# Kernel optimization log

Measured on AMD Instinct MI355X. Metric: run time of the kernel, lower is better.

Reference implementation:

```python
import jax, jax.numpy as jnp
import numpy as np
from itertools import combinations

A = 4          # anchor_points
K = 16         # neighbor_num
INTRA = A * (A - 1) // 2   # 6
CH = INTRA * 2 + A * A     # 28 = generator channels
B, N, S = 1, 8192, 4096
CIN, COUT = 64, 128


def cdist(x):
    # pairwise euclidean distances [B,N,N], zero-safe sqrt (zero grad at d=0)
    sq = jnp.sum(x * x, -1)
    d2 = sq[:, :, None] + sq[:, None, :] - 2.0 * jnp.einsum('bnc,bmc->bnm', x, x)
    d2 = jnp.maximum(d2, 0.0)
    m = d2 > 0
    return jnp.where(m, jnp.sqrt(jnp.where(m, d2, 1.0)), 0.0)


def index_points(points, idx):
    # points [B,N,...], idx [B,*] -> [B,*,...]
    return jax.vmap(lambda p, i: p[i])(points, idx)


def index_points_dists(dists, i1, i2):
    # dists [B,N,N]; result[b,...] = dists[b, i1[b,...], i2[b,...]]
    i1, i2 = jnp.broadcast_arrays(i1, i2)
    return jax.vmap(lambda d, a, b: d[a, b])(dists, i1, i2)


def generator(xyz):
    # RotationInvariantDistFea.forward(xyz, concat_raw_relative_fea=True)
    D = cdist(xyz)
    neg_nd, ni = jax.lax.top_k(-D, K)   # K >= A; smallest-K, sorted ascending
    nd = -neg_nd
    ai = ni[:, :, :A]
    # intra-anchor dists: dists to anchors 1..A-1 plus pairwise dists among them
    subs = [index_points_dists(D, ai[:, :, pi], ai[:, :, pj])[:, :, None]
            for pi, pj in combinations(range(1, A), 2)]
    intra = jnp.concatenate([nd[:, :, 1:A]] + subs, axis=2)  # [B,P,6]
    # inter-anchor dists: center anchors x neighbor anchors -> [B,P,K,A*A]
    nai = index_points(ai, ni)                                # [B,P,K,A]
    inter = index_points_dists(D, ai[:, :, None, :, None],
                               nai[:, :, :, None, :]).reshape(D.shape[0], D.shape[1], K, A * A)
    center = jnp.broadcast_to(intra[:, :, None, :], (intra.shape[0], intra.shape[1], K, INTRA))
    rf = jnp.concatenate([center, index_points(intra, ni), inter], axis=3)  # [B,P,K,28]
    return rf, ni, D


def mlp(x, W, b, g, be, act):
    # Linear + BatchNorm1d (training mode: stats over batch*points) + optional leaky_relu(0.2)
    y = x @ W + b
    mu = jnp.mean(y, (0, 1))
    var = jnp.var(y, (0, 1))
    y = (y - mu) * jax.lax.rsqrt(var + 1e-5) * g + be
    return jax.nn.leaky_relu(y, 0.2) if act else y


def forward(xyz, feature, sample_indexes, Ww, bw, gw, betaw, Wb, bb, gb, betab, Wo, bo, go, betao):
    rf_before, ni_before, D_before = generator(xyz)
    intra_before = rf_before[:, :, 0, :INTRA]
    xyz_s = index_points(xyz, sample_indexes)
    feat = index_points(feature, sample_indexes)
    intra_before = index_points(intra_before, sample_indexes)
    rf_after, ni_after, _ = generator(xyz_s)
    intra_after = rf_after[:, :, 0, :INTRA]
    a_before = index_points(ni_before[:, :, :A], sample_indexes)                  # [B,S,A]
    a_after = jax.vmap(lambda s, a: s[a])(sample_indexes, ni_after[:, :, :A])     # map to global idx
    inter = index_points_dists(D_before, a_before[:, :, :, None],
                               a_after[:, :, None, :]).reshape(B, S, A * A)
    adf = jnp.concatenate([intra_before, intra_after, inter], axis=2)             # [B,S,28]
    w = mlp(adf, Ww, bw, gw, betaw, False)
    bia = mlp(adf, Wb, bb, gb, betab, False)
    feat = jax.nn.leaky_relu(feat * w + bia, 0.2)
    feat = jnp.concatenate([feat, adf], axis=2)                                   # [B,S,92]
    feat = mlp(feat, Wo, bo, go, betao, True)                                     # [B,S,128]
    return xyz_s, feat, rf_after, ni_after


def setup_inputs():
    key = jax.random.key(0)
    ks = jax.random.split(key, 8)
    xyz = jax.random.normal(ks[0], (B, N, 3), jnp.float32)
    feature = jax.random.normal(ks[1], (B, N, CIN), jnp.float32)
    sample_indexes = jnp.stack([jax.random.permutation(jax.random.fold_in(ks[2], i), N)[:S]
                                for i in range(B)]).astype(jnp.int32)

    def lin(k, cin, cout):
        k1, k2 = jax.random.split(k)
        W = jax.random.normal(k1, (cin, cout), jnp.float32) / np.float32(np.sqrt(cin))
        b = jax.random.normal(k2, (cout,), jnp.float32) * 0.01
        return W, b, jnp.ones((cout,), jnp.float32), jnp.zeros((cout,), jnp.float32)

    Ww, bw, gw, betaw = lin(ks[5], CH, CIN)
    Wb, bb, gb, betab = lin(ks[6], CH, CIN)
    Wo, bo, go, betao = lin(ks[7], CH + CIN, COUT)
    return dict(xyz=xyz, feature=feature, sample_indexes=sample_indexes,
                Ww=Ww, bw=bw, gw=gw, betaw=betaw,
                Wb=Wb, bb=bb, gb=gb, betab=betab,
                Wo=Wo, bo=bo, go=go, betao=betao)


def reference(xyz, feature, sample_indexes, Ww, bw, gw, betaw, Wb, bb, gb, betab, Wo, bo, go, betao):
    return forward(xyz, feature, sample_indexes, Ww, bw, gw, betaw, Wb, bb, gb, betab, Wo, bo, go, betao)
```

## Files before the change

kernel.cpp:

```cpp
#include <hip/hip_runtime.h>
#include <hip/hip_bf16.h>
#include <math.h>

#define N_PTS 8192
#define S_PTS 4096
typedef unsigned long long u64;
typedef unsigned u32;

__device__ __forceinline__ float pair_dist_d(const float4 a, const float4 b) {
    double ax = a.x, ay = a.y, az = a.z;
    double bx = b.x, by = b.y, bz = b.z;
    double dx = ax - bx, dy = ay - by, dz = az - bz;
    double d2 = dx * dx + dy * dy + dz * dz;
    return d2 > 0.0 ? (float)sqrt(d2) : 0.0f;
}

__device__ __forceinline__ float d2_f32_gram(const float4 a, const float4 b) {
    float dot = __fadd_rn(__fadd_rn(__fmul_rn(a.x, b.x), __fmul_rn(a.y, b.y)),
                          __fmul_rn(a.z, b.z));
    float d2 = __fsub_rn(__fadd_rn(a.w, b.w), __fmul_rn(2.0f, dot));
    return fmaxf(d2, 0.0f);
}

__global__ __launch_bounds__(256) void stage_kernel(
        const float* __restrict__ xyz, const int* __restrict__ sidx,
        float4* __restrict__ cb, float4* __restrict__ ca,
        float* __restrict__ out_xyz_s) {
    int i = blockIdx.x * blockDim.x + threadIdx.x;
    if (i < N_PTS) {
        float x = xyz[i * 3 + 0], y = xyz[i * 3 + 1], z = xyz[i * 3 + 2];
        float sq = __fadd_rn(__fadd_rn(__fmul_rn(x, x), __fmul_rn(y, y)),
                             __fmul_rn(z, z));
        cb[i] = make_float4(x, y, z, sq);
    }
    if (i < S_PTS) {
        int si = sidx[i];
        float x = xyz[si * 3 + 0], y = xyz[si * 3 + 1], z = xyz[si * 3 + 2];
        float sq = __fadd_rn(__fadd_rn(__fmul_rn(x, x), __fmul_rn(y, y)),
                             __fmul_rn(z, z));
        ca[i] = make_float4(x, y, z, sq);
        out_xyz_s[i * 3 + 0] = x;
        out_xyz_s[i * 3 + 1] = y;
        out_xyz_s[i * 3 + 2] = z;
    }
}


template <int KOUT, int ITERS>
__device__ u64 knn_full_ladder(const float4 q, const float4* __restrict__ cand,
                               int lane) {
    u32 Lk[KOUT], Li[KOUT];
#pragma unroll
    for (int j = 0; j < KOUT; ++j) { Lk[j] = 0xFFFFFFFFu; Li[j] = 0xFFFFFFFFu; }
    int c = lane;
    for (int tt = 0; tt < ITERS; ++tt, c += 64) {
        float d2 = d2_f32_gram(q, cand[c]);
        float Df = d2 > 0.0f ? __fsqrt_rn(d2) : 0.0f;
        u32 kb = __float_as_uint(Df);
        if (kb < Lk[KOUT - 1]) {
#pragma unroll
            for (int j = KOUT - 1; j >= 1; --j) {
                bool up = kb < Lk[j - 1], ins = kb < Lk[j];
                Lk[j] = up ? Lk[j - 1] : (ins ? kb : Lk[j]);
                Li[j] = up ? Li[j - 1] : (ins ? (u32)c : Li[j]);
            }
            bool i0 = kb < Lk[0];
            Lk[0] = i0 ? kb : Lk[0];
            Li[0] = i0 ? (u32)c : Li[0];
        }
    }
    u64 Lu[KOUT];
#pragma unroll
    for (int j = 0; j < KOUT; ++j) Lu[j] = ((u64)Lk[j] << 32) | (u64)Li[j];
    u64 res = ~0ull;
#pragma unroll
    for (int r = 0; r < KOUT; ++r) {
        u64 m = Lu[0];
#pragma unroll
        for (int off = 32; off >= 1; off >>= 1) {
            u64 o = __shfl_xor(m, off, 64);
            m = (o < m) ? o : m;
        }
        if (lane == r) res = m;
        if (Lu[0] == m) {
#pragma unroll
            for (int j = 0; j < KOUT - 1; ++j) Lu[j] = Lu[j + 1];
            Lu[KOUT - 1] = ~0ull;
        }
    }
    return res;
}

template <int J, int K, int NC>
__device__ u64 knn_select(const float4 q, const float4* __restrict__ cand,
                          int t, u32* mins, u64* buf, u32* shm) {
    int lane = t & 63, wid = t >> 6;
    u32 d2b[J];
    u32 m = 0xFFFFFFFFu;
#pragma unroll
    for (int j = 0; j < J; ++j) {
        float d2 = d2_f32_gram(q, cand[t + 256 * j]);
        u32 b = __float_as_uint(d2);
        d2b[j] = b;
        m = b < m ? b : m;
    }
    mins[t] = m;
    __syncthreads();
    if (wid == 0) {
        u32 v = mins[lane];
        u32 v2 = mins[lane + 64];  v = v2 < v ? v2 : v;
        v2 = mins[lane + 128];     v = v2 < v ? v2 : v;
        v2 = mins[lane + 192];     v = v2 < v ? v2 : v;
#pragma unroll
        for (int k = 2; k <= 64; k <<= 1) {
#pragma unroll
            for (int j2 = k >> 1; j2 >= 1; j2 >>= 1) {
                u32 o = __shfl_xor(v, j2, 64);
                bool keepMin = (((lane & j2) == 0) == ((lane & k) == 0));
                bool less = o < v;
                v = keepMin ? (less ? o : v) : (less ? v : o);
            }
        }
        if (lane == K - 1) shm[0] = v;
    }
    __syncthreads();
    u32 tau = shm[0];
    u32 c = 0;
#pragma unroll
    for (int j = 0; j < J; ++j) c += (d2b[j] <= tau) ? 1u : 0u;
    u32 x = c;
#pragma unroll
    for (int off = 1; off < 64; off <<= 1) {
        u32 y = __shfl_up(x, off, 64);
        if (lane >= off) x += y;
    }
    if (lane == 63) shm[1 + wid] = x;
    __syncthreads();
    u32 base = x - c;
    for (int w = 0; w < wid; ++w) base += shm[1 + w];
    u32 cnt = shm[1] + shm[2] + shm[3] + shm[4];
    if (cnt <= 256u) {
        u32 off = base;
#pragma unroll
        for (int j = 0; j < J; ++j) {
            if (d2b[j] <= tau) {
                float d2 = __uint_as_float(d2b[j]);
                float D = d2 > 0.0f ? __fsqrt_rn(d2) : 0.0f;
                buf[off++] = ((u64)__float_as_uint(D) << 32) |
                             (u64)(u32)(t + 256 * j);
            }
        }
    }
    __syncthreads();
    u64 res = ~0ull;
    if (wid == 0) {
        if (cnt <= 64u) {
            u64 v = (lane < (int)cnt) ? buf[lane] : ~0ull;
#pragma unroll
            for (int k = 2; k <= 64; k <<= 1) {
#pragma unroll
                for (int j2 = k >> 1; j2 >= 1; j2 >>= 1) {
                    u64 o = __shfl_xor(v, j2, 64);
                    bool keepMin = (((lane & j2) == 0) == ((lane & k) == 0));
                    bool less = o < v;
                    v = keepMin ? (less ? o : v) : (less ? v : o);
                }
            }
            res = v;
        } else if (cnt <= 256u) {
            u64 L0 = ~0ull, L1 = ~0ull, L2 = ~0ull, L3 = ~0ull;
            for (u32 mm = lane; mm < cnt; mm += 64) {
                u64 kk = buf[mm];
                if (kk < L3) {
                    if (kk < L1) {
                        L3 = L2; L2 = L1;
                        if (kk < L0) { L1 = L0; L0 = kk; } else L1 = kk;
                    } else {
                        if (kk < L2) { L3 = L2; L2 = kk; } else L3 = kk;
                    }
                }
            }
#pragma unroll
            for (int r = 0; r < K; ++r) {
                u64 mr = L0;
#pragma unroll
                for (int off = 32; off >= 1; off >>= 1) {
                    u64 o = __shfl_xor(mr, off, 64);
                    mr = (o < mr) ? o : mr;
                }
                if (lane == r) res = mr;
                if (L0 == mr) { L0 = L1; L1 = L2; L2 = L3; L3 = ~0ull; }
            }
        } else {
            res = knn_full_ladder<K, NC / 64>(q, cand, lane);
        }
    }
    return res;
}

__global__ __launch_bounds__(256, 4) void knn_kernel(
        const float4* __restrict__ cb, const float4* __restrict__ ca,
        const int* __restrict__ sidx,
        int* __restrict__ a_before, float* __restrict__ intra_before,
        int* __restrict__ ni_i, float* __restrict__ intra_after,
        float* __restrict__ out_ni) {
    __shared__ u32 mins[256];
    __shared__ u64 buf[256];
    __shared__ u32 shm[8];
    int t = threadIdx.x, lane = t & 63, wid = t >> 6;
    int bid = blockIdx.x;
    if (bid < S_PTS) {
        int s = bid;
        float4 q = ca[s];
        u64 res = knn_select<16, 16, 4096>(q, ca, t, mins, buf, shm);
        if (wid == 0) {
            int idx = (int)(res & 0xffffffffull);
            if (lane < 16) {
                ni_i[s * 16 + lane] = idx;
                out_ni[s * 16 + lane] = (float)idx;
            }
            if (lane >= 1 && lane < 4)
                intra_after[s * 6 + (lane - 1)] = pair_dist_d(q, ca[idx]);
            int i1 = __shfl(idx, 1, 64);
            int i2 = __shfl(idx, 2, 64);
            int i3 = __shfl(idx, 3, 64);
            if (lane < 3) {
                int pa = (lane == 2) ? i2 : i1;
                int pb = (lane == 0) ? i2 : i3;
                intra_after[s * 6 + 3 + lane] = pair_dist_d(ca[pa], ca[pb]);
            }
        }
    } else {
        int s = bid - S_PTS;
        float4 q = cb[sidx[s]];
        u64 res = knn_select<32, 4, 8192>(q, cb, t, mins, buf, shm);
        if (wid == 0) {
            int idx = (int)(res & 0xffffffffull);
            if (lane < 4) a_before[s * 4 + lane] = idx;
            if (lane >= 1 && lane < 4)
                intra_before[s * 6 + (lane - 1)] = pair_dist_d(q, cb[idx]);
            int i1 = __shfl(idx, 1, 64);
            int i2 = __shfl(idx, 2, 64);
            int i3 = __shfl(idx, 3, 64);
            if (lane < 3) {
                int pa = (lane == 2) ? i2 : i1;
                int pb = (lane == 0) ? i2 : i3;
                intra_before[s * 6 + 3 + lane] = pair_dist_d(cb[pa], cb[pb]);
            }
        }
    }
}

__global__ __launch_bounds__(256) void assemble_kernel(
        const float4* __restrict__ ca, const float4* __restrict__ cb,
        const int* __restrict__ ni_i, const float* __restrict__ intra_after,
        const int* __restrict__ a_before, const float* __restrict__ intra_before,
        const int* __restrict__ sidx,
        float* __restrict__ out_rf, float* __restrict__ adf) {
    __shared__ int s_ni[4][16];
    __shared__ float s_rf[4][16 * 28];
    __shared__ float s_ia[4][8];
    int t = threadIdx.x, wid = t >> 6, lane = t & 63;
    int s = blockIdx.x * 4 + wid;
    if (lane < 16) s_ni[wid][lane] = ni_i[s * 16 + lane];
    if (lane < 6) s_ia[wid][lane] = intra_after[s * 6 + lane];
    __syncthreads();

    int k = lane >> 2, qq = lane & 3;
    int nai_q = ni_i[s_ni[wid][k] * 16 + qq];
    float4 pq = ca[nai_q];
#pragma unroll
    for (int p = 0; p < 4; ++p) {
        float4 pp = ca[s_ni[wid][p]];
        s_rf[wid][k * 28 + 12 + p * 4 + qq] = pair_dist_d(pp, pq);
    }
    for (int idx = lane; idx < 16 * 12; idx += 64) {
        int kk = idx / 12, c = idx % 12;
        float v = (c < 6) ? s_ia[wid][c] : intra_after[s_ni[wid][kk] * 6 + (c - 6)];
        s_rf[wid][kk * 28 + c] = v;
    }
    if (lane < 16) {
        int p = lane >> 2, q2 = lane & 3;
        int ib = a_before[s * 4 + p];
        int ia = sidx[s_ni[wid][q2]];
        adf[s * 28 + 12 + lane] = pair_dist_d(cb[ib], cb[ia]);
    } else if (lane >= 32 && lane < 38) {
        adf[s * 28 + (lane - 32)] = intra_before[s * 6 + (lane - 32)];
    } else if (lane >= 40 && lane < 46) {
        adf[s * 28 + 6 + (lane - 40)] = s_ia[wid][lane - 40];
    }
    __syncthreads();
    const int base = s * 16 * 28;
    for (int idx = lane; idx < 16 * 28; idx += 64) out_rf[base + idx] = s_rf[wid][idx];
}

__global__ __launch_bounds__(256) void mlp1_kernel(
        const float* __restrict__ adf,
        const float* __restrict__ Ww, const float* __restrict__ bw,
        const float* __restrict__ Wb, const float* __restrict__ bb,
        float* __restrict__ y_wb) {
    __shared__ float sW[28 * 128];
    __shared__ float sb[128];
    __shared__ float sA[32 * 28];
    int t = threadIdx.x;
    for (int i = t; i < 28 * 128; i += 256) {
        int k = i >> 7, c = i & 127;
        sW[i] = (c < 64) ? Ww[k * 64 + c] : Wb[k * 64 + (c - 64)];
    }
    if (t < 128) sb[t] = (t < 64) ? bw[t] : bb[t - 64];
    int s0 = blockIdx.x * 32;
    for (int i = t; i < 32 * 28; i += 256) sA[i] = adf[s0 * 28 + i];
    __syncthreads();
    int sl = t >> 3, grp = t & 7;
    int s = s0 + sl;
    float acc[16];
#pragma unroll
    for (int k = 0; k < 16; ++k) acc[k] = sb[grp * 16 + k];
    for (int k2 = 0; k2 < 28; ++k2) {
        float a = sA[sl * 28 + k2];
#pragma unroll
        for (int k = 0; k < 16; ++k)
            acc[k] = fmaf(a, sW[k2 * 128 + grp * 16 + k], acc[k]);
    }
#pragma unroll
    for (int k = 0; k < 16; ++k) y_wb[(grp * 16 + k) * 4096 + s] = acc[k];
}

__global__ __launch_bounds__(256) void stats_kernel(
        const float* __restrict__ y,
        const float* __restrict__ g0, const float* __restrict__ be0,
        const float* __restrict__ g1, const float* __restrict__ be1, int csplit,
        float* __restrict__ scale, float* __restrict__ shift) {
    int c = blockIdx.x;
    const float* p = y + c * 4096;
    float s1 = 0.0f, s2 = 0.0f;
    for (int i = threadIdx.x; i < 4096; i += 256) {
        float v = p[i];
        s1 += v;
        s2 = fmaf(v, v, s2);
    }
    __shared__ float l1[256], l2[256];
    l1[threadIdx.x] = s1;
    l2[threadIdx.x] = s2;
    __syncthreads();
    for (int off = 128; off; off >>= 1) {
        if (threadIdx.x < off) {
            l1[threadIdx.x] += l1[threadIdx.x + off];
            l2[threadIdx.x] += l2[threadIdx.x + off];
        }
        __syncthreads();
    }
    if (threadIdx.x == 0) {
        float mean = l1[0] * (1.0f / 4096.0f);
        float var = l2[0] * (1.0f / 4096.0f) - mean * mean;
        float g = (c < csplit) ? g0[c] : g1[c - csplit];
        float be = (c < csplit) ? be0[c] : be1[c - csplit];
        float sc = g / sqrtf(var + 1e-5f);
        scale[c] = sc;
        shift[c] = be - mean * sc;
    }
}

__global__ __launch_bounds__(256) void mlp2_kernel(
        const float* __restrict__ y_wb,
        const float* __restrict__ scale1, const float* __restrict__ shift1,
        const float* __restrict__ feature, const int* __restrict__ sidx,
        const float* __restrict__ adf,
        const float* __restrict__ Wo, const float* __restrict__ bo,
        float* __restrict__ y_o) {
    __shared__ float sW[92 * 128];
    __shared__ float t2[16 * 129];
    __shared__ float scat[16 * 92];
    int t = threadIdx.x;
    int s0 = blockIdx.x * 16;
    for (int i = t; i < 92 * 128; i += 256) sW[i] = Wo[i];
    for (int i = t; i < 16 * 128; i += 256) {
        int row = i & 15, c = i >> 4;
        t2[row * 129 + c] = fmaf(y_wb[c * 4096 + s0 + row], scale1[c], shift1[c]);
    }
    __syncthreads();
    for (int rr = 0; rr < 16; rr += 4) {
        int r = rr + (t >> 6);
        int c = t & 63;
        int si = sidx[s0 + r];
        float f = feature[si * 64 + c];
        float v = fmaf(f, t2[r * 129 + c], t2[r * 129 + 64 + c]);
        scat[r * 92 + c] = v >= 0.0f ? v : 0.2f * v;
    }
    for (int i = t; i < 16 * 28; i += 256) {
        int row = i / 28, k = i % 28;
        scat[row * 92 + 64 + k] = adf[(s0 + row) * 28 + k];
    }
    __syncthreads();
    int r = t >> 4, cg = t & 15;
    float acc[8];
#pragma unroll
    for (int j = 0; j < 8; ++j) acc[j] = bo[cg * 8 + j];
    for (int c = 0; c < 92; ++c) {
        float a = scat[r * 92 + c];
#pragma unroll
        for (int j = 0; j < 8; ++j)
            acc[j] = fmaf(a, sW[c * 128 + cg * 8 + j], acc[j]);
    }
    int s = s0 + r;
#pragma unroll
    for (int j = 0; j < 8; ++j) y_o[(cg * 8 + j) * 4096 + s] = acc[j];
}

__global__ __launch_bounds__(256) void final_kernel(
        const float* __restrict__ y_o,
        const float* __restrict__ scale, const float* __restrict__ shift,
        float* __restrict__ out_feat) {
    int tid = blockIdx.x * 256 + threadIdx.x;
    int j = tid >> 12;
    int s = tid & 4095;
    float v = fmaf(y_o[tid], scale[j], shift[j]);
    v = v >= 0.0f ? v : 0.2f * v;
    out_feat[s * 128 + j] = v;
}

extern "C" void kernel_launch(void* const* d_in, const int* in_sizes, int n_in,
                              void* d_out, int out_size, void* d_ws, size_t ws_size,
                              hipStream_t stream) {
    const float* xyz = (const float*)d_in[0];
    const float* feature = (const float*)d_in[1];
    const int* sidx = (const int*)d_in[2];
    const float* Ww = (const float*)d_in[3];
    const float* bw = (const float*)d_in[4];
    const float* gw = (const float*)d_in[5];
    const float* betaw = (const float*)d_in[6];
    const float* Wb = (const float*)d_in[7];
    const float* bb = (const float*)d_in[8];
    const float* gb = (const float*)d_in[9];
    const float* betab = (const float*)d_in[10];
    const float* Wo = (const float*)d_in[11];
    const float* bo = (const float*)d_in[12];
    const float* go = (const float*)d_in[13];
    const float* betao = (const float*)d_in[14];

    float* out = (float*)d_out;
    float* out_xyz = out;
    float* out_feat = out + 12288;
    float* out_rf = out + 12288 + 524288;
    float* out_ni = out + 12288 + 524288 + 1835008;

    float* ws = (float*)d_ws;
    float4* cb = (float4*)ws;
    float4* ca = (float4*)(ws + 32768);
    int* a_before = (int*)(ws + 49152);
    float* intra_before = ws + 65536;
    int* ni_i = (int*)(ws + 90112);
    float* intra_after = ws + 155648;
    float* adf = ws + 180224;
    float* y_wb = ws + 294912;
    float* y_o = ws + 819200;
    float* scale1 = ws + 1343488;
    float* shift1 = ws + 1343616;
    float* scale_o = ws + 1343744;
    float* shift_o = ws + 1343872;

    stage_kernel<<<32, 256, 0, stream>>>(xyz, sidx, cb, ca, out_xyz);
    knn_kernel<<<2 * S_PTS, 256, 0, stream>>>(cb, ca, sidx, a_before, intra_before,
                                              ni_i, intra_after, out_ni);
    assemble_kernel<<<1024, 256, 0, stream>>>(ca, cb, ni_i, intra_after, a_before,
                                              intra_before, sidx, out_rf, adf);
    mlp1_kernel<<<128, 256, 0, stream>>>(adf, Ww, bw, Wb, bb, y_wb);
    stats_kernel<<<128, 256, 0, stream>>>(y_wb, gw, betaw, gb, betab, 64, scale1, shift1);
    mlp2_kernel<<<256, 256, 0, stream>>>(y_wb, scale1, shift1, feature, sidx, adf, Wo, bo, y_o);
    stats_kernel<<<128, 256, 0, stream>>>(y_o, go, betao, go, betao, 128, scale_o, shift_o);
    final_kernel<<<2048, 256, 0, stream>>>(y_o, scale_o, shift_o, out_feat);
}
```

Measured before the change: 171.5 us.

## Merge before/after kNN into one 8192-candidate pass per query pair, fuse kernels

The kNN kernel now handles two sampled queries per block and scans all 8192 points once. Both the before-sampling top-4 and the after-sampling top-16 are derived from that single scan, with the sampled subset identified through an inverse-index map built in the stage kernel. This removes the separate scan over the 4096 sampled points. Assembly is fused with the first MLP, and the second stats pass is fused into the final kernel, cutting launches and intermediate traffic. The trade-offs are heavier register pressure (64 distance registers per thread), a cold fallback ladder that now gathers through the inverse map, an added memset, and final-kernel output writes strided by 128.

```diff
diff --git a/kernel.cpp b/kernel.cpp
--- a/kernel.cpp
+++ b/kernel.cpp
@@ -22,10 +22,38 @@
     return fmaxf(d2, 0.0f);
 }
 
+__device__ __forceinline__ u32 bitonic64_u32(u32 v, int lane) {
+#pragma unroll
+    for (int k = 2; k <= 64; k <<= 1) {
+#pragma unroll
+        for (int j2 = k >> 1; j2 >= 1; j2 >>= 1) {
+            u32 o = __shfl_xor(v, j2, 64);
+            bool keepMin = (((lane & j2) == 0) == ((lane & k) == 0));
+            bool less = o < v;
+            v = keepMin ? (less ? o : v) : (less ? v : o);
+        }
+    }
+    return v;
+}
+
+__device__ __forceinline__ u64 bitonic64_u64(u64 v, int lane) {
+#pragma unroll
+    for (int k = 2; k <= 64; k <<= 1) {
+#pragma unroll
+        for (int j2 = k >> 1; j2 >= 1; j2 >>= 1) {
+            u64 o = __shfl_xor(v, j2, 64);
+            bool keepMin = (((lane & j2) == 0) == ((lane & k) == 0));
+            bool less = o < v;
+            v = keepMin ? (less ? o : v) : (less ? v : o);
+        }
+    }
+    return v;
+}
+
 __global__ __launch_bounds__(256) void stage_kernel(
         const float* __restrict__ xyz, const int* __restrict__ sidx,
         float4* __restrict__ cb, float4* __restrict__ ca,
-        float* __restrict__ out_xyz_s) {
+        int* __restrict__ inv, float* __restrict__ out_xyz_s) {
     int i = blockIdx.x * blockDim.x + threadIdx.x;
     if (i < N_PTS) {
         float x = xyz[i * 3 + 0], y = xyz[i * 3 + 1], z = xyz[i * 3 + 2];
@@ -39,229 +67,237 @@
         float sq = __fadd_rn(__fadd_rn(__fmul_rn(x, x), __fmul_rn(y, y)),
                              __fmul_rn(z, z));
         ca[i] = make_float4(x, y, z, sq);
+        inv[si] = i;
         out_xyz_s[i * 3 + 0] = x;
         out_xyz_s[i * 3 + 1] = y;
         out_xyz_s[i * 3 + 2] = z;
     }
 }
 
-
-template <int KOUT, int ITERS>
-__device__ u64 knn_full_ladder(const float4 q, const float4* __restrict__ cand,
-                               int lane) {
-    u32 Lk[KOUT], Li[KOUT];
-#pragma unroll
-    for (int j = 0; j < KOUT; ++j) { Lk[j] = 0xFFFFFFFFu; Li[j] = 0xFFFFFFFFu; }
-    int c = lane;
-    for (int tt = 0; tt < ITERS; ++tt, c += 64) {
-        float d2 = d2_f32_gram(q, cand[c]);
-        float Df = d2 > 0.0f ? __fsqrt_rn(d2) : 0.0f;
-        u32 kb = __float_as_uint(Df);
-        if (kb < Lk[KOUT - 1]) {
-#pragma unroll
-            for (int j = KOUT - 1; j >= 1; --j) {
-                bool up = kb < Lk[j - 1], ins = kb < Lk[j];
-                Lk[j] = up ? Lk[j - 1] : (ins ? kb : Lk[j]);
-                Li[j] = up ? Li[j - 1] : (ins ? (u32)c : Li[j]);
-            }
-            bool i0 = kb < Lk[0];
-            Lk[0] = i0 ? kb : Lk[0];
-            Li[0] = i0 ? (u32)c : Li[0];
-        }
-    }
-    u64 Lu[KOUT];
-#pragma unroll
-    for (int j = 0; j < KOUT; ++j) Lu[j] = ((u64)Lk[j] << 32) | (u64)Li[j];
+template <int K, bool AFTER>
+__device__ u64 cold_ladder(const float4 q, const float4* __restrict__ cb,
+                           const int* __restrict__ inv, int lane) {
+    u64 L[K];
+#pragma unroll
+    for (int j = 0; j < K; ++j) L[j] = ~0ull;
+    for (int c = lane; c < N_PTS; c += 64) {
+        int low = c;
+        bool ok = true;
+        if (AFTER) { int iv = inv[c]; ok = iv >= 0; low = iv; }
+        if (!ok) continue;
+        float d2 = d2_f32_gram(q, cb[c]);
+        float D = d2 > 0.0f ? __fsqrt_rn(d2) : 0.0f;
+        u64 key = ((u64)__float_as_uint(D) << 32) | (u64)(u32)low;
+        if (key < L[K - 1]) {
+#pragma unroll
+            for (int j = K - 1; j >= 1; --j)
+                L[j] = (key < L[j - 1]) ? L[j - 1] : ((key < L[j]) ? key : L[j]);
+            L[0] = (key < L[0]) ? key : L[0];
+        }
+    }
     u64 res = ~0ull;
 #pragma unroll
-    for (int r = 0; r < KOUT; ++r) {
-        u64 m = Lu[0];
+    for (int r = 0; r < K; ++r) {
+        u64 m = L[0];
 #pragma unroll
         for (int off = 32; off >= 1; off >>= 1) {
             u64 o = __shfl_xor(m, off, 64);
             m = (o < m) ? o : m;
         }
         if (lane == r) res = m;
-        if (Lu[0] == m) {
-#pragma unroll
-            for (int j = 0; j < KOUT - 1; ++j) Lu[j] = Lu[j + 1];
-            Lu[KOUT - 1] = ~0ull;
+        if (L[0] == m) {
+#pragma unroll
+            for (int j = 0; j < K - 1; ++j) L[j] = L[j + 1];
+            L[K - 1] = ~0ull;
         }
     }
     return res;
 }
 
-template <int J, int K, int NC>
-__device__ u64 knn_select(const float4 q, const float4* __restrict__ cand,
-                          int t, u32* mins, u64* buf, u32* shm) {
-    int lane = t & 63, wid = t >> 6;
-    u32 d2b[J];
-    u32 m = 0xFFFFFFFFu;
-#pragma unroll
-    for (int j = 0; j < J; ++j) {
-        float d2 = d2_f32_gram(q, cand[t + 256 * j]);
-        u32 b = __float_as_uint(d2);
-        d2b[j] = b;
-        m = b < m ? b : m;
-    }
-    mins[t] = m;
-    __syncthreads();
-    if (wid == 0) {
-        u32 v = mins[lane];
-        u32 v2 = mins[lane + 64];  v = v2 < v ? v2 : v;
-        v2 = mins[lane + 128];     v = v2 < v ? v2 : v;
-        v2 = mins[lane + 192];     v = v2 < v ? v2 : v;
-#pragma unroll
-        for (int k = 2; k <= 64; k <<= 1) {
-#pragma unroll
-            for (int j2 = k >> 1; j2 >= 1; j2 >>= 1) {
-                u32 o = __shfl_xor(v, j2, 64);
-                bool keepMin = (((lane & j2) == 0) == ((lane & k) == 0));
-                bool less = o < v;
-                v = keepMin ? (less ? o : v) : (less ? v : o);
+template <int K>
+__device__ u64 finalize_sort(const u64* buf, u32 cnt, int lane) {
+    if (cnt <= 64u) {
+        u64 v = (lane < (int)cnt) ? buf[lane] : ~0ull;
+        return bitonic64_u64(v, lane);
+    }
+    u64 L0 = ~0ull, L1 = ~0ull, L2 = ~0ull, L3 = ~0ull;
+    for (u32 mm = lane; mm < cnt; mm += 64) {
+        u64 kk = buf[mm];
+        if (kk < L3) {
+            if (kk < L1) {
+                L3 = L2; L2 = L1;
+                if (kk < L0) { L1 = L0; L0 = kk; } else L1 = kk;
+            } else {
+                if (kk < L2) { L3 = L2; L2 = kk; } else L3 = kk;
             }
         }
-        if (lane == K - 1) shm[0] = v;
-    }
-    __syncthreads();
-    u32 tau = shm[0];
-    u32 c = 0;
-#pragma unroll
-    for (int j = 0; j < J; ++j) c += (d2b[j] <= tau) ? 1u : 0u;
-    u32 x = c;
-#pragma unroll
-    for (int off = 1; off < 64; off <<= 1) {
-        u32 y = __shfl_up(x, off, 64);
-        if (lane >= off) x += y;
-    }
-    if (lane == 63) shm[1 + wid] = x;
-    __syncthreads();
-    u32 base = x - c;
-    for (int w = 0; w < wid; ++w) base += shm[1 + w];
-    u32 cnt = shm[1] + shm[2] + shm[3] + shm[4];
-    if (cnt <= 256u) {
-        u32 off = base;
-#pragma unroll
-        for (int j = 0; j < J; ++j) {
-            if (d2b[j] <= tau) {
-                float d2 = __uint_as_float(d2b[j]);
-                float D = d2 > 0.0f ? __fsqrt_rn(d2) : 0.0f;
-                buf[off++] = ((u64)__float_as_uint(D) << 32) |
-                             (u64)(u32)(t + 256 * j);
-            }
-        }
-    }
-    __syncthreads();
+    }
     u64 res = ~0ull;
-    if (wid == 0) {
-        if (cnt <= 64u) {
-            u64 v = (lane < (int)cnt) ? buf[lane] : ~0ull;
-#pragma unroll
-            for (int k = 2; k <= 64; k <<= 1) {
-#pragma unroll
-                for (int j2 = k >> 1; j2 >= 1; j2 >>= 1) {
-                    u64 o = __shfl_xor(v, j2, 64);
-                    bool keepMin = (((lane & j2) == 0) == ((lane & k) == 0));
-                    bool less = o < v;
-                    v = keepMin ? (less ? o : v) : (less ? v : o);
-                }
-            }
-            res = v;
-        } else if (cnt <= 256u) {
-            u64 L0 = ~0ull, L1 = ~0ull, L2 = ~0ull, L3 = ~0ull;
-            for (u32 mm = lane; mm < cnt; mm += 64) {
-                u64 kk = buf[mm];
-                if (kk < L3) {
-                    if (kk < L1) {
-                        L3 = L2; L2 = L1;
-                        if (kk < L0) { L1 = L0; L0 = kk; } else L1 = kk;
-                    } else {
-                        if (kk < L2) { L3 = L2; L2 = kk; } else L3 = kk;
-                    }
-                }
-            }
-#pragma unroll
-            for (int r = 0; r < K; ++r) {
-                u64 mr = L0;
-#pragma unroll
-                for (int off = 32; off >= 1; off >>= 1) {
-                    u64 o = __shfl_xor(mr, off, 64);
-                    mr = (o < mr) ? o : mr;
-                }
-                if (lane == r) res = mr;
-                if (L0 == mr) { L0 = L1; L1 = L2; L2 = L3; L3 = ~0ull; }
-            }
-        } else {
-            res = knn_full_ladder<K, NC / 64>(q, cand, lane);
-        }
+#pragma unroll
+    for (int r = 0; r < K; ++r) {
+        u64 mr = L0;
+#pragma unroll
+        for (int off = 32; off >= 1; off >>= 1) {
+            u64 o = __shfl_xor(mr, off, 64);
+            mr = (o < mr) ? o : mr;
+        }
+        if (lane == r) res = mr;
+        if (L0 == mr) { L0 = L1; L1 = L2; L2 = L3; L3 = ~0ull; }
     }
     return res;
 }
 
 __global__ __launch_bounds__(256, 4) void knn_kernel(
         const float4* __restrict__ cb, const float4* __restrict__ ca,
-        const int* __restrict__ sidx,
+        const int* __restrict__ inv, const int* __restrict__ sidx,
         int* __restrict__ a_before, float* __restrict__ intra_before,
         int* __restrict__ ni_i, float* __restrict__ intra_after,
         float* __restrict__ out_ni) {
-    __shared__ u32 mins[256];
-    __shared__ u64 buf[256];
-    __shared__ u32 shm[8];
+    __shared__ u32 smin[4][256];
+    __shared__ u64 sbuf[4][256];
+    __shared__ u32 staus[4];
+    __shared__ u32 stot[2][4];
     int t = threadIdx.x, lane = t & 63, wid = t >> 6;
-    int bid = blockIdx.x;
-    if (bid < S_PTS) {
-        int s = bid;
-        float4 q = ca[s];
-        u64 res = knn_select<16, 16, 4096>(q, ca, t, mins, buf, shm);
-        if (wid == 0) {
-            int idx = (int)(res & 0xffffffffull);
-            if (lane < 16) {
-                ni_i[s * 16 + lane] = idx;
-                out_ni[s * 16 + lane] = (float)idx;
-            }
-            if (lane >= 1 && lane < 4)
-                intra_after[s * 6 + (lane - 1)] = pair_dist_d(q, ca[idx]);
-            int i1 = __shfl(idx, 1, 64);
-            int i2 = __shfl(idx, 2, 64);
-            int i3 = __shfl(idx, 3, 64);
-            if (lane < 3) {
-                int pa = (lane == 2) ? i2 : i1;
-                int pb = (lane == 0) ? i2 : i3;
-                intra_after[s * 6 + 3 + lane] = pair_dist_d(ca[pa], ca[pb]);
-            }
+    int s0 = blockIdx.x * 2, s1 = s0 + 1;
+    float4 q0 = cb[sidx[s0]], q1 = cb[sidx[s1]];
+
+    u32 d20[32], d21[32], msk = 0;
+    u32 mnA0 = ~0u, mnA1 = ~0u, mnS0 = ~0u, mnS1 = ~0u;
+#pragma unroll
+    for (int j = 0; j < 32; ++j) {
+        int c = t + 256 * j;
+        float4 p = cb[c];
+        u32 b0 = __float_as_uint(d2_f32_gram(q0, p));
+        u32 b1 = __float_as_uint(d2_f32_gram(q1, p));
+        d20[j] = b0; d21[j] = b1;
+        bool smp = inv[c] >= 0;
+        msk |= (u32)smp << j;
+        mnA0 = b0 < mnA0 ? b0 : mnA0;
+        mnA1 = b1 < mnA1 ? b1 : mnA1;
+        mnS0 = (smp && b0 < mnS0) ? b0 : mnS0;
+        mnS1 = (smp && b1 < mnS1) ? b1 : mnS1;
+    }
+    smin[0][t] = mnA0; smin[1][t] = mnA1; smin[2][t] = mnS0; smin[3][t] = mnS1;
+    __syncthreads();
+    {
+        u32 v = smin[wid][lane];
+        u32 v2 = smin[wid][lane + 64];  v = v2 < v ? v2 : v;
+        v2 = smin[wid][lane + 128];     v = v2 < v ? v2 : v;
+        v2 = smin[wid][lane + 192];     v = v2 < v ? v2 : v;
+        v = bitonic64_u32(v, lane);
+        int kk = (wid < 2) ? 3 : 15;
+        if (lane == kk) staus[wid] = v;
+    }
+    __syncthreads();
+    u32 tb0 = staus[0], tb1 = staus[1], ta0 = staus[2], ta1 = staus[3];
+    u32 p0 = 0, p1 = 0;
+#pragma unroll
+    for (int j = 0; j < 32; ++j) {
+        u32 sm = (msk >> j) & 1u;
+        p0 += ((d20[j] <= tb0) ? 0x10000u : 0u) + ((sm && d20[j] <= ta0) ? 1u : 0u);
+        p1 += ((d21[j] <= tb1) ? 0x10000u : 0u) + ((sm && d21[j] <= ta1) ? 1u : 0u);
+    }
+    u32 x0 = p0, x1 = p1;
+#pragma unroll
+    for (int off = 1; off < 64; off <<= 1) {
+        u32 y0 = __shfl_up(x0, off, 64);
+        u32 y1 = __shfl_up(x1, off, 64);
+        if (lane >= off) { x0 += y0; x1 += y1; }
+    }
+    if (lane == 63) { stot[0][wid] = x0; stot[1][wid] = x1; }
+    __syncthreads();
+    u32 b0s = x0 - p0, b1s = x1 - p1;
+    for (int w = 0; w < wid; ++w) { b0s += stot[0][w]; b1s += stot[1][w]; }
+    u32 tot0 = stot[0][0] + stot[0][1] + stot[0][2] + stot[0][3];
+    u32 tot1 = stot[1][0] + stot[1][1] + stot[1][2] + stot[1][3];
+    u32 cntB0 = tot0 >> 16, cntA0 = tot0 & 0xFFFFu;
+    u32 cntB1 = tot1 >> 16, cntA1 = tot1 & 0xFFFFu;
+    u32 ob0 = b0s >> 16, oa0 = b0s & 0xFFFFu;
+    u32 ob1 = b1s >> 16, oa1 = b1s & 0xFFFFu;
+#pragma unroll
+    for (int j = 0; j < 32; ++j) {
+        int c = t + 256 * j;
+        u32 sm = (msk >> j) & 1u;
+        bool qb0 = d20[j] <= tb0, qa0 = sm && d20[j] <= ta0;
+        if (qb0 || qa0) {
+            float d2v = __uint_as_float(d20[j]);
+            float D = d2v > 0.0f ? __fsqrt_rn(d2v) : 0.0f;
+            u64 hk = (u64)__float_as_uint(D) << 32;
+            if (qb0 && cntB0 <= 256u) sbuf[0][ob0++] = hk | (u64)(u32)c;
+            if (qa0 && cntA0 <= 256u) sbuf[2][oa0++] = hk | (u64)(u32)inv[c];
+        }
+        bool qb1 = d21[j] <= tb1, qa1 = sm && d21[j] <= ta1;
+        if (qb1 || qa1) {
+            float d2v = __uint_as_float(d21[j]);
+            float D = d2v > 0.0f ? __fsqrt_rn(d2v) : 0.0f;
+            u64 hk = (u64)__float_as_uint(D) << 32;
+            if (qb1 && cntB1 <= 256u) sbuf[1][ob1++] = hk | (u64)(u32)c;
+            if (qa1 && cntA1 <= 256u) sbuf[3][oa1++] = hk | (u64)(u32)inv[c];
+        }
+    }
+    __syncthreads();
+    int s = (wid & 1) ? s1 : s0;
+    float4 q = (wid & 1) ? q1 : q0;
+    u32 cnt = (wid == 0) ? cntB0 : (wid == 1) ? cntB1 : (wid == 2) ? cntA0 : cntA1;
+    u64 res;
+    if (wid < 2) {
+        res = (cnt <= 256u) ? finalize_sort<4>(sbuf[wid], cnt, lane)
+                            : cold_ladder<4, false>(q, cb, inv, lane);
+        int idx = (int)(res & 0xffffffffull);
+        if (lane < 4) a_before[s * 4 + lane] = idx;
+        if (lane >= 1 && lane < 4)
+            intra_before[s * 6 + (lane - 1)] = pair_dist_d(q, cb[idx]);
+        int i1 = __shfl(idx, 1, 64);
+        int i2 = __shfl(idx, 2, 64);
+        int i3 = __shfl(idx, 3, 64);
+        if (lane < 3) {
+            int pa = (lane == 2) ? i2 : i1;
+            int pb = (lane == 0) ? i2 : i3;
+            intra_before[s * 6 + 3 + lane] = pair_dist_d(cb[pa], cb[pb]);
         }
     } else {
-        int s = bid - S_PTS;
-        float4 q = cb[sidx[s]];
-        u64 res = knn_select<32, 4, 8192>(q, cb, t, mins, buf, shm);
-        if (wid == 0) {
-            int idx = (int)(res & 0xffffffffull);
-            if (lane < 4) a_before[s * 4 + lane] = idx;
-            if (lane >= 1 && lane < 4)
-                intra_before[s * 6 + (lane - 1)] = pair_dist_d(q, cb[idx]);
-            int i1 = __shfl(idx, 1, 64);
-            int i2 = __shfl(idx, 2, 64);
-            int i3 = __shfl(idx, 3, 64);
-            if (lane < 3) {
-                int pa = (lane == 2) ? i2 : i1;
-                int pb = (lane == 0) ? i2 : i3;
-                intra_before[s * 6 + 3 + lane] = pair_dist_d(cb[pa], cb[pb]);
-            }
-        }
-    }
-}
-
-__global__ __launch_bounds__(256) void assemble_kernel(
+        res = (cnt <= 256u) ? finalize_sort<16>(sbuf[wid], cnt, lane)
+                            : cold_ladder<16, true>(q, cb, inv, lane);
+        int idx = (int)(res & 0xffffffffull);
+        if (lane < 16) {
+            ni_i[s * 16 + lane] = idx;
+            out_ni[s * 16 + lane] = (float)idx;
+        }
+        if (lane >= 1 && lane < 4)
+            intra_after[s * 6 + (lane - 1)] = pair_dist_d(q, ca[idx]);
+        int i1 = __shfl(idx, 1, 64);
+        int i2 = __shfl(idx, 2, 64);
+        int i3 = __shfl(idx, 3, 64);
+        if (lane < 3) {
+            int pa = (lane == 2) ? i2 : i1;
+            int pb = (lane == 0) ? i2 : i3;
+            intra_after[s * 6 + 3 + lane] = pair_dist_d(ca[pa], ca[pb]);
+        }
+    }
+}
+
+__global__ __launch_bounds__(256) void asm_mlp1_kernel(
         const float4* __restrict__ ca, const float4* __restrict__ cb,
         const int* __restrict__ ni_i, const float* __restrict__ intra_after,
         const int* __restrict__ a_before, const float* __restrict__ intra_before,
         const int* __restrict__ sidx,
-        float* __restrict__ out_rf, float* __restrict__ adf) {
+        const float* __restrict__ Ww, const float* __restrict__ bw,
+        const float* __restrict__ Wb, const float* __restrict__ bb,
+        float* __restrict__ out_rf, float* __restrict__ adf,
+        float* __restrict__ y_wb) {
     __shared__ int s_ni[4][16];
     __shared__ float s_rf[4][16 * 28];
     __shared__ float s_ia[4][8];
+    __shared__ float s_adf[4][28];
+    __shared__ float sW[28 * 128];
+    __shared__ float sb[128];
     int t = threadIdx.x, wid = t >> 6, lane = t & 63;
     int s = blockIdx.x * 4 + wid;
+    for (int i = t; i < 28 * 128; i += 256) {
+        int k = i >> 7, c = i & 127;
+        sW[i] = (c < 64) ? Ww[k * 64 + c] : Wb[k * 64 + (c - 64)];
+    }
+    if (t < 128) sb[t] = (t < 64) ? bw[t] : bb[t - 64];
     if (lane < 16) s_ni[wid][lane] = ni_i[s * 16 + lane];
     if (lane < 6) s_ia[wid][lane] = intra_after[s * 6 + lane];
     __syncthreads();
@@ -283,47 +319,31 @@
         int p = lane >> 2, q2 = lane & 3;
         int ib = a_before[s * 4 + p];
         int ia = sidx[s_ni[wid][q2]];
-        adf[s * 28 + 12 + lane] = pair_dist_d(cb[ib], cb[ia]);
+        float v = pair_dist_d(cb[ib], cb[ia]);
+        adf[s * 28 + 12 + lane] = v;
+        s_adf[wid][12 + lane] = v;
     } else if (lane >= 32 && lane < 38) {
-        adf[s * 28 + (lane - 32)] = intra_before[s * 6 + (lane - 32)];
+        float v = intra_before[s * 6 + (lane - 32)];
+        adf[s * 28 + (lane - 32)] = v;
+        s_adf[wid][lane - 32] = v;
     } else if (lane >= 40 && lane < 46) {
-        adf[s * 28 + 6 + (lane - 40)] = s_ia[wid][lane - 40];
-    }
-    __syncthreads();
+        float v = s_ia[wid][lane - 40];
+        adf[s * 28 + 6 + (lane - 40)] = v;
+        s_adf[wid][6 + (lane - 40)] = v;
+    }
     const int base = s * 16 * 28;
     for (int idx = lane; idx < 16 * 28; idx += 64) out_rf[base + idx] = s_rf[wid][idx];
-}
-
-__global__ __launch_bounds__(256) void mlp1_kernel(
-        const float* __restrict__ adf,
-        const float* __restrict__ Ww, const float* __restrict__ bw,
-        const float* __restrict__ Wb, const float* __restrict__ bb,
-        float* __restrict__ y_wb) {
-    __shared__ float sW[28 * 128];
-    __shared__ float sb[128];
-    __shared__ float sA[32 * 28];
-    int t = threadIdx.x;
-    for (int i = t; i < 28 * 128; i += 256) {
-        int k = i >> 7, c = i & 127;
-        sW[i] = (c < 64) ? Ww[k * 64 + c] : Wb[k * 64 + (c - 64)];
-    }
-    if (t < 128) sb[t] = (t < 64) ? bw[t] : bb[t - 64];
-    int s0 = blockIdx.x * 32;
-    for (int i = t; i < 32 * 28; i += 256) sA[i] = adf[s0 * 28 + i];
-    __syncthreads();
-    int sl = t >> 3, grp = t & 7;
-    int s = s0 + sl;
-    float acc[16];
-#pragma unroll
-    for (int k = 0; k < 16; ++k) acc[k] = sb[grp * 16 + k];
-    for (int k2 = 0; k2 < 28; ++k2) {
-        float a = sA[sl * 28 + k2];
-#pragma unroll
-        for (int k = 0; k < 16; ++k)
-            acc[k] = fmaf(a, sW[k2 * 128 + grp * 16 + k], acc[k]);
-    }
-#pragma unroll
-    for (int k = 0; k < 16; ++k) y_wb[(grp * 16 + k) * 4096 + s] = acc[k];
+    __syncthreads();
+    int s0 = blockIdx.x * 4;
+#pragma unroll
+    for (int o = t; o < 512; o += 256) {
+        int r = o >> 7, c = o & 127;
+        float acc = sb[c];
+#pragma unroll
+        for (int k2 = 0; k2 < 28; ++k2)
+            acc = fmaf(s_adf[r][k2], sW[k2 * 128 + c], acc);
+        y_wb[c * 4096 + s0 + r] = acc;
+    }
 }
 
 __global__ __launch_bounds__(256) void stats_kernel(
@@ -409,14 +429,42 @@
 
 __global__ __launch_bounds__(256) void final_kernel(
         const float* __restrict__ y_o,
-        const float* __restrict__ scale, const float* __restrict__ shift,
+        const float* __restrict__ go, const float* __restrict__ betao,
         float* __restrict__ out_feat) {
-    int tid = blockIdx.x * 256 + threadIdx.x;
-    int j = tid >> 12;
-    int s = tid & 4095;
-    float v = fmaf(y_o[tid], scale[j], shift[j]);
-    v = v >= 0.0f ? v : 0.2f * v;
-    out_feat[s * 128 + j] = v;
+    int j = blockIdx.x;
+    const float* p = y_o + j * 4096;
+    float s1 = 0.0f, s2 = 0.0f;
+    for (int i = threadIdx.x; i < 4096; i += 256) {
+        float v = p[i];
+        s1 += v;
+        s2 = fmaf(v, v, s2);
+    }
+    __shared__ float l1[256], l2[256];
+    __shared__ float ssc, ssh;
+    l1[threadIdx.x] = s1;
+    l2[threadIdx.x] = s2;
+    __syncthreads();
+    for (int off = 128; off; off >>= 1) {
+        if (threadIdx.x < off) {
+            l1[threadIdx.x] += l1[threadIdx.x + off];
+            l2[threadIdx.x] += l2[threadIdx.x + off];
+        }
+        __syncthreads();
+    }
+    if (threadIdx.x == 0) {
+        float mean = l1[0] * (1.0f / 4096.0f);
+        float var = l2[0] * (1.0f / 4096.0f) - mean * mean;
+        float sc = go[j] / sqrtf(var + 1e-5f);
+        ssc = sc;
+        ssh = betao[j] - mean * sc;
+    }
+    __syncthreads();
+    float sc = ssc, sh = ssh;
+    for (int i = threadIdx.x; i < 4096; i += 256) {
+        float v = fmaf(p[i], sc, sh);
+        v = v >= 0.0f ? v : 0.2f * v;
+        out_feat[i * 128 + j] = v;
+    }
 }
 
 extern "C" void kernel_launch(void* const* d_in, const int* in_sizes, int n_in,
@@ -456,17 +504,16 @@
     float* y_o = ws + 819200;
     float* scale1 = ws + 1343488;
     float* shift1 = ws + 1343616;
-    float* scale_o = ws + 1343744;
-    float* shift_o = ws + 1343872;
-
-    stage_kernel<<<32, 256, 0, stream>>>(xyz, sidx, cb, ca, out_xyz);
-    knn_kernel<<<2 * S_PTS, 256, 0, stream>>>(cb, ca, sidx, a_before, intra_before,
-                                              ni_i, intra_after, out_ni);
-    assemble_kernel<<<1024, 256, 0, stream>>>(ca, cb, ni_i, intra_after, a_before,
-                                              intra_before, sidx, out_rf, adf);
-    mlp1_kernel<<<128, 256, 0, stream>>>(adf, Ww, bw, Wb, bb, y_wb);
+    int* inv = (int*)(ws + 1343744);
+
+    hipMemsetAsync(inv, 0xFF, N_PTS * sizeof(int), stream);
+    stage_kernel<<<32, 256, 0, stream>>>(xyz, sidx, cb, ca, inv, out_xyz);
+    knn_kernel<<<2048, 256, 0, stream>>>(cb, ca, inv, sidx, a_before, intra_before,
+                                         ni_i, intra_after, out_ni);
+    asm_mlp1_kernel<<<1024, 256, 0, stream>>>(ca, cb, ni_i, intra_after, a_before,
+                                              intra_before, sidx, Ww, bw, Wb, bb,
+                                              out_rf, adf, y_wb);
     stats_kernel<<<128, 256, 0, stream>>>(y_wb, gw, betaw, gb, betab, 64, scale1, shift1);
     mlp2_kernel<<<256, 256, 0, stream>>>(y_wb, scale1, shift1, feature, sidx, adf, Wo, bo, y_o);
-    stats_kernel<<<128, 256, 0, stream>>>(y_o, go, betao, go, betao, 128, scale_o, shift_o);
-    final_kernel<<<2048, 256, 0, stream>>>(y_o, scale_o, shift_o, out_feat);
-}
+    final_kernel<<<128, 256, 0, stream>>>(y_o, go, betao, out_feat);
+}
```

Result: slower. 198.8 us (+16.0%).
